# Optimization experiments

Hardware: AMD Instinct MI355X
Metric: run time of the kernel (lower is better)

## Reference

```python
import jax, jax.numpy as jnp
import numpy as np
from jax import lax

B, L, F, H, K = 16, 512, 384, 384, 3
MAX_OUT = 4096  # static upper bound on sum of durations (L * (fill_max-1) = 3584)
EPS = 1e-5
PAD = K // 2


def setup_inputs() -> dict:
    key = jax.random.key(0)
    ks = jax.random.split(key, 6)
    s = 0.02
    return {
        "input": jax.random.normal(ks[0], (B, L, F), jnp.float32),
        "target": jax.random.randint(ks[1], (B, L), 0, 8, jnp.int32),
        "conv1_w": jax.random.normal(ks[2], (H, F, K), jnp.float32) * s,
        "conv1_b": jnp.zeros((H,), jnp.float32),
        "ln1_g": jnp.ones((H,), jnp.float32),
        "ln1_b": jnp.zeros((H,), jnp.float32),
        "conv2_w": jax.random.normal(ks[3], (F, H, K), jnp.float32) * s,
        "conv2_b": jnp.zeros((F,), jnp.float32),
        "ln2_g": jnp.ones((F,), jnp.float32),
        "ln2_b": jnp.zeros((F,), jnp.float32),
        "lin_w": jax.random.normal(ks[4], (F, 1), jnp.float32) * s,
        "lin_b": jnp.zeros((1,), jnp.float32),
    }


def _conv1d(x, w, b):
    # x: [B, L, Cin] -> [B, L, Cout]; w: [Cout, Cin, K] (torch Conv1d layout)
    y = lax.conv_general_dilated(
        x.transpose(0, 2, 1), w, window_strides=(1,), padding=[(PAD, PAD)],
        dimension_numbers=("NCH", "OIH", "NCH"))
    return y.transpose(0, 2, 1) + b


def _layer_norm(x, g, b):
    mu = jnp.mean(x, axis=-1, keepdims=True)
    var = jnp.mean(jnp.square(x - mu), axis=-1, keepdims=True)
    return (x - mu) * lax.rsqrt(var + EPS) * g + b


def _length_regulate(x, dur_int):
    # cumsum-based index mapping + gather (vectorized LR_function)
    ends = jnp.cumsum(dur_int, axis=-1)                      # [B, L]
    ts = jnp.arange(MAX_OUT)                                 # [T]
    idx = jax.vmap(lambda e: jnp.searchsorted(e, ts, side="right"))(ends)  # [B, T]
    gathered = jnp.take_along_axis(x, jnp.clip(idx, 0, L - 1)[:, :, None], axis=1)
    mask = (ts[None, :] < ends[:, -1:]).astype(x.dtype)      # zero-pad past total length
    return gathered * mask[:, :, None]


def reference(input, target, conv1_w, conv1_b, ln1_g, ln1_b,
              conv2_w, conv2_b, ln2_g, ln2_b, lin_w, lin_b):
    # DurationPredictor (eval mode: dropout is identity)
    h = jax.nn.relu(_layer_norm(_conv1d(input, conv1_w, conv1_b), ln1_g, ln1_b))
    h = jax.nn.relu(_layer_norm(_conv1d(h, conv2_w, conv2_b), ln2_g, ln2_b))
    durations = jnp.exp(jax.nn.relu(h @ lin_w + lin_b))       # [B, L, 1]
    # LR_function with target durations (round of int target is identity)
    out = _length_regulate(input, target)                      # [B, MAX_OUT, F]
    return out, durations
```

## Files before the change

### kernel.cpp

```cpp
#include <hip/hip_runtime.h>
#include <math.h>

#define B_ 16
#define L_ 512
#define F_ 384
#define H_ 384
#define K_ 3
#define MAX_OUT_ 4096
#define EPS_ 1e-5f

#define M_TOTAL (B_ * L_)
#define KDIM (K_ * F_)
#define NMB 128
#define NCG 6
#define NST 36
#define APANEL (66 * 64)
#define AMBLK (12 * APANEL)
#define APLANE (NMB * AMBLK)
#define BSTEP 4096
#define BCG (NST * BSTEP)
#define BPLANE (NCG * BCG)

typedef __attribute__((ext_vector_type(8))) short bf16x8;
typedef __attribute__((ext_vector_type(4))) float f32x4;

__device__ inline unsigned short bf16_rne(float v) {
    unsigned int u = __float_as_uint(v);
    unsigned int r = (u + 0x7fffu + ((u >> 16) & 1u)) >> 16;
    return (unsigned short)r;
}
__device__ inline void bf16_split(float v, unsigned short& hi, unsigned short& lo) {
    hi = bf16_rne(v);
    float hf = __uint_as_float(((unsigned int)hi) << 16);
    lo = bf16_rne(v - hf);
}

__global__ void k_scan_prep(const int* __restrict__ target, int* __restrict__ idx,
                            const float* __restrict__ x,
                            const float* __restrict__ w1, const float* __restrict__ w2,
                            unsigned short* __restrict__ aph, unsigned short* __restrict__ apl,
                            unsigned short* __restrict__ b1h, unsigned short* __restrict__ b1l,
                            unsigned short* __restrict__ b2h, unsigned short* __restrict__ b2l) {
    if (blockIdx.x < 16) {
        __shared__ int e[L_];
        const int b = blockIdx.x;
        const int tid = threadIdx.x;
        e[tid] = target[b * L_ + tid];
        __syncthreads();
        for (int off = 1; off < L_; off <<= 1) {
            int add = (tid >= off) ? e[tid - off] : 0;
            __syncthreads();
            e[tid] += add;
            __syncthreads();
        }
        const int total = e[L_ - 1];
        for (int t = tid; t < MAX_OUT_; t += L_) {
            int lo = 0, hi = L_;
            while (lo < hi) {
                int m = (lo + hi) >> 1;
                if (e[m] <= t) lo = m + 1; else hi = m;
            }
            int v = (t < total) ? min(lo, L_ - 1) : -1;
            idx[b * MAX_OUT_ + t] = v;
        }
        return;
    }
    const int NA8 = NMB * 12 * 66 * 4;
    const int NB8 = NCG * NST * 64 * 4;
    const int total = NA8 + 2 * NB8;
    for (int i = (blockIdx.x - 16) * blockDim.x + threadIdx.x; i < total;
         i += (gridDim.x - 16) * blockDim.x) {
        if (i < NA8) {
            const int m = i / 3168;
            int r1 = i - m * 3168;
            const int fs = r1 / 264;
            int r2 = r1 - fs * 264;
            const int rp = r2 >> 2;
            const int p = r2 & 3;
            const int cgk = p ^ ((rp >> 1) & 3);
            const int f0 = fs * 32 + cgk * 8;
            const int ll = ((m & 7) << 6) + rp - 1;
            ushort4 h0 = {0,0,0,0}, h1 = {0,0,0,0}, l0 = {0,0,0,0}, l1 = {0,0,0,0};
            if (ll >= 0 && ll < L_) {
                const float* src = x + ((size_t)((m >> 3) * L_ + ll) * F_ + f0);
                float4 va = ((const float4*)src)[0];
                float4 vb = ((const float4*)src)[1];
                bf16_split(va.x, h0.x, l0.x); bf16_split(va.y, h0.y, l0.y);
                bf16_split(va.z, h0.z, l0.z); bf16_split(va.w, h0.w, l0.w);
                bf16_split(vb.x, h1.x, l1.x); bf16_split(vb.y, h1.y, l1.y);
                bf16_split(vb.z, h1.z, l1.z); bf16_split(vb.w, h1.w, l1.w);
            }
            ((ushort4*)aph)[i * 2] = h0;  ((ushort4*)aph)[i * 2 + 1] = h1;
            ((ushort4*)apl)[i * 2] = l0;  ((ushort4*)apl)[i * 2 + 1] = l1;
        } else {
            int j = i - NA8;
            const int conv = j / NB8;
            int j2 = j - conv * NB8;
            const float* w = conv ? w2 : w1;
            unsigned short* bh = conv ? b2h : b1h;
            unsigned short* bl = conv ? b2l : b1l;
            const int cg = j2 / 9216;
            int r1 = j2 - cg * 9216;
            const int s = r1 / 256;
            int r2 = r1 - s * 256;
            const int rc = r2 >> 2;
            const int p = r2 & 3;
            const int tap = s / 12;
            const int fs = s - tap * 12;
            const int cgk = p ^ ((rc >> 1) & 3);
            const int f0 = fs * 32 + cgk * 8;
            const int h = cg * 64 + rc;
            ushort4 hv0, hv1, lv0, lv1;
            unsigned short th, tl;
#define WSPLIT(E, DH, DL) bf16_split(w[(size_t)(h * F_ + f0 + (E)) * K_ + tap], th, tl); DH = th; DL = tl;
            WSPLIT(0, hv0.x, lv0.x) WSPLIT(1, hv0.y, lv0.y)
            WSPLIT(2, hv0.z, lv0.z) WSPLIT(3, hv0.w, lv0.w)
            WSPLIT(4, hv1.x, lv1.x) WSPLIT(5, hv1.y, lv1.y)
            WSPLIT(6, hv1.z, lv1.z) WSPLIT(7, hv1.w, lv1.w)
#undef WSPLIT
            ((ushort4*)bh)[j2 * 2] = hv0;  ((ushort4*)bh)[j2 * 2 + 1] = hv1;
            ((ushort4*)bl)[j2 * 2] = lv0;  ((ushort4*)bl)[j2 * 2 + 1] = lv1;
        }
    }
}

typedef __attribute__((address_space(3))) char lds_char;
typedef const __attribute__((address_space(1))) char g_char;

#define GLDS(gsrc, ldst)                                                   \
    __builtin_amdgcn_global_load_lds((g_char*)(gsrc), (lds_char*)(ldst), 16, 0, 0)

#define ST(S) {                                                            \
    const int off = wvA ? ((((S) % 12) * 66 + (S) / 12) * 64) : ((S) * 4096); \
    _Pragma("unroll")                                                      \
    for (int q = 0; q < 4; ++q)                                            \
        GLDS(srcbase + off + q * 1024,                                     \
             smem + ((S) % 3) * 16384 + wvoff + q * 1024);                 \
}

#define MFMA1(A, Bv, MI, NI)                                               \
    acc[MI][NI] = __builtin_amdgcn_mfma_f32_16x16x32_bf16(A, Bv, acc[MI][NI], 0, 0, 0);

#define STEP(S, NW, DOSTAGE) {                                             \
    asm volatile("s_waitcnt vmcnt(" #NW ")" ::: "memory");                 \
    __builtin_amdgcn_s_barrier();                                          \
    const char* bb = smem + ((S) % 3) * 16384;                             \
    const int tp = (S) / 12;                                               \
    bf16x8 ah0 = *(const bf16x8*)(bb + aadr0[tp]);                         \
    bf16x8 ah1 = *(const bf16x8*)(bb + aadr1[tp]);                         \
    bf16x8 al0 = *(const bf16x8*)(bb + 4096 + aadr0[tp]);                  \
    bf16x8 al1 = *(const bf16x8*)(bb + 4096 + aadr1[tp]);                  \
    bf16x8 bh0 = *(const bf16x8*)(bb + 8192 + badr0);                      \
    bf16x8 bh1 = *(const bf16x8*)(bb + 8192 + badr1);                      \
    bf16x8 bl0 = *(const bf16x8*)(bb + 12288 + badr0);                     \
    bf16x8 bl1 = *(const bf16x8*)(bb + 12288 + badr1);                     \
    DOSTAGE;                                                               \
    asm volatile("s_waitcnt lgkmcnt(0)" ::: "memory");                     \
    __builtin_amdgcn_sched_barrier(0);                                     \
    __builtin_amdgcn_s_setprio(1);                                         \
    MFMA1(ah0, bh0, 0, 0) MFMA1(ah0, bh1, 0, 1)                            \
    MFMA1(ah1, bh0, 1, 0) MFMA1(ah1, bh1, 1, 1)                            \
    MFMA1(ah0, bl0, 0, 0) MFMA1(ah0, bl1, 0, 1)                            \
    MFMA1(ah1, bl0, 1, 0) MFMA1(ah1, bl1, 1, 1)                            \
    MFMA1(al0, bh0, 0, 0) MFMA1(al0, bh1, 0, 1)                            \
    MFMA1(al1, bh0, 1, 0) MFMA1(al1, bh1, 1, 1)                            \
    __builtin_amdgcn_s_setprio(0);                                         \
}

__global__ __launch_bounds__(256, 3) void k_gemm(
        const unsigned short* __restrict__ Aph,
        const unsigned short* __restrict__ Apl,
        const unsigned short* __restrict__ Bph,
        const unsigned short* __restrict__ Bpl,
        float* __restrict__ C) {
    __shared__ __align__(1024) char smem[49152];
    const int lane = threadIdx.x & 63;
    const int wv = threadIdx.x >> 6;
    const int wr = wv >> 1;
    const int wc = wv & 1;
    const int m = blockIdx.x;
    const int cg = blockIdx.y;
    const int r0 = m * 64;
    const int h0 = cg * 64;

    const bool wvA = (wv < 2);
    const int wvoff = wv * 4096;
    const char* srcbase;
    {
        const char* ap = (wv == 0) ? (const char*)Aph : (const char*)Apl;
        const char* bp = (wv == 2) ? (const char*)Bph : (const char*)Bpl;
        srcbase = (wvA ? ap + (size_t)m * AMBLK : bp + (size_t)cg * BCG) + lane * 16;
    }

    const int fr = lane & 15;
    const int fc = lane >> 4;
    const int rowA0 = wr * 32 + fr, rowA1 = rowA0 + 16;
    const int colB0 = wc * 32 + fr, colB1 = colB0 + 16;
    int aadr0[3], aadr1[3];
#pragma unroll
    for (int t = 0; t < 3; ++t) {
        aadr0[t] = rowA0 * 64 + ((fc ^ (((rowA0 + t) >> 1) & 3)) << 4);
        aadr1[t] = rowA1 * 64 + ((fc ^ (((rowA1 + t) >> 1) & 3)) << 4);
    }
    const int badr0 = colB0 * 64 + ((fc ^ ((colB0 >> 1) & 3)) << 4);
    const int badr1 = colB1 * 64 + ((fc ^ ((colB1 >> 1) & 3)) << 4);

    const f32x4 z4 = {0.f, 0.f, 0.f, 0.f};
    f32x4 acc[2][2];
    acc[0][0] = z4; acc[0][1] = z4; acc[1][0] = z4; acc[1][1] = z4;

    ST(0) ST(1)

    STEP(0, 4, ST(2))   STEP(1, 4, ST(3))   STEP(2, 4, ST(4))
    STEP(3, 4, ST(5))   STEP(4, 4, ST(6))   STEP(5, 4, ST(7))
    STEP(6, 4, ST(8))   STEP(7, 4, ST(9))   STEP(8, 4, ST(10))
    STEP(9, 4, ST(11))  STEP(10, 4, ST(12)) STEP(11, 4, ST(13))
    STEP(12, 4, ST(14)) STEP(13, 4, ST(15)) STEP(14, 4, ST(16))
    STEP(15, 4, ST(17)) STEP(16, 4, ST(18)) STEP(17, 4, ST(19))
    STEP(18, 4, ST(20)) STEP(19, 4, ST(21)) STEP(20, 4, ST(22))
    STEP(21, 4, ST(23)) STEP(22, 4, ST(24)) STEP(23, 4, ST(25))
    STEP(24, 4, ST(26)) STEP(25, 4, ST(27)) STEP(26, 4, ST(28))
    STEP(27, 4, ST(29)) STEP(28, 4, ST(30)) STEP(29, 4, ST(31))
    STEP(30, 4, ST(32)) STEP(31, 4, ST(33)) STEP(32, 4, ST(34))
    STEP(33, 4, ST(35)) STEP(34, 4, )       STEP(35, 0, )

    const int rb = (lane >> 4) * 4;
#pragma unroll
    for (int mi = 0; mi < 2; ++mi)
#pragma unroll
        for (int ni = 0; ni < 2; ++ni)
#pragma unroll
            for (int r = 0; r < 4; ++r)
                C[(size_t)(r0 + wr * 32 + mi * 16 + rb + r) * H_ +
                  h0 + wc * 32 + ni * 16 + fr] = acc[mi][ni][r];
}

__global__ __launch_bounds__(256) void k_lnrelu(
        const float* __restrict__ c, const float* __restrict__ cb,
        const float* __restrict__ g, const float* __restrict__ bt,
        unsigned short* __restrict__ oh, unsigned short* __restrict__ ol) {
    const int row = blockIdx.x * 4 + (threadIdx.x >> 6);
    const int lane = threadIdx.x & 63;
    const float* cr = c + (size_t)row * H_;
    float2 dv[3];
    dv[0] = ((const float2*)cr)[lane];
    dv[1] = ((const float2*)cr)[lane + 64];
    dv[2] = ((const float2*)cr)[lane + 128];
#pragma unroll
    for (int p = 0; p < 3; ++p) {
        const int ch = 2 * (lane + 64 * p);
        dv[p].x += cb[ch];
        dv[p].y += cb[ch + 1];
    }
    float s = dv[0].x + dv[0].y + dv[1].x + dv[1].y + dv[2].x + dv[2].y;
    float s2 = dv[0].x * dv[0].x + dv[0].y * dv[0].y + dv[1].x * dv[1].x
             + dv[1].y * dv[1].y + dv[2].x * dv[2].x + dv[2].y * dv[2].y;
    for (int off = 32; off >= 1; off >>= 1) {
        s += __shfl_xor(s, off);
        s2 += __shfl_xor(s2, off);
    }
    const float mu = s * (1.f / H_);
    const float var = s2 * (1.f / H_) - mu * mu;
    const float rs = rsqrtf(var + EPS_);
    unsigned short hv[6], lv[6];
#pragma unroll
    for (int p = 0; p < 3; ++p) {
        const int ch = 2 * (lane + 64 * p);
        float r0 = fmaxf((dv[p].x - mu) * rs * g[ch] + bt[ch], 0.f);
        float r1 = fmaxf((dv[p].y - mu) * rs * g[ch + 1] + bt[ch + 1], 0.f);
        bf16_split(r0, hv[2 * p], lv[2 * p]);
        bf16_split(r1, hv[2 * p + 1], lv[2 * p + 1]);
    }
#define WSLOT(M, RP) {                                                        \
    _Pragma("unroll")                                                         \
    for (int p = 0; p < 3; ++p) {                                             \
        const int ch = 2 * (lane + 64 * p);                                   \
        const int fs = ch >> 5;                                               \
        const int k32 = ch & 31;                                              \
        const int pst = (k32 >> 3) ^ (((RP) >> 1) & 3);                       \
        const size_t ix = ((size_t)(((M) * 12 + fs) * 66 + (RP)) * 4 + pst) * 8 + (k32 & 7); \
        *(ushort2*)(oh + ix) = make_ushort2(hv[2 * p], hv[2 * p + 1]);        \
        *(ushort2*)(ol + ix) = make_ushort2(lv[2 * p], lv[2 * p + 1]);        \
    }                                                                         \
}
    const int m1 = row >> 6;
    const int rsub = row & 63;
    WSLOT(m1, rsub + 1);
    if (rsub == 0 && (row & 511) != 0)   WSLOT(m1 - 1, 65);
    if (rsub == 63 && (row & 511) != 511) WSLOT(m1 + 1, 0);
#undef WSLOT
}

__global__ __launch_bounds__(256) void k_fin_gather(
        const float* __restrict__ c, const float* __restrict__ cb,
        const float* __restrict__ g, const float* __restrict__ bt,
        const float* __restrict__ lw, const float* __restrict__ lb,
        float* __restrict__ dur,
        const float4* __restrict__ x, const int* __restrict__ idx,
        float4* __restrict__ out) {
    if (blockIdx.x < 2048) {
        const int row = blockIdx.x * 4 + (threadIdx.x >> 6);
        const int lane = threadIdx.x & 63;
        const float* cr = c + (size_t)row * F_;
        float2 dv[3];
        dv[0] = ((const float2*)cr)[lane];
        dv[1] = ((const float2*)cr)[lane + 64];
        dv[2] = ((const float2*)cr)[lane + 128];
#pragma unroll
        for (int p = 0; p < 3; ++p) {
            const int ch = 2 * (lane + 64 * p);
            dv[p].x += cb[ch];
            dv[p].y += cb[ch + 1];
        }
        float s = dv[0].x + dv[0].y + dv[1].x + dv[1].y + dv[2].x + dv[2].y;
        float s2 = dv[0].x * dv[0].x + dv[0].y * dv[0].y + dv[1].x * dv[1].x
                 + dv[1].y * dv[1].y + dv[2].x * dv[2].x + dv[2].y * dv[2].y;
        for (int off = 32; off >= 1; off >>= 1) {
            s += __shfl_xor(s, off);
            s2 += __shfl_xor(s2, off);
        }
        const float mu = s * (1.f / F_);
        const float var = s2 * (1.f / F_) - mu * mu;
        const float rs = rsqrtf(var + EPS_);
        float dot = 0.f;
#pragma unroll
        for (int p = 0; p < 3; ++p) {
            const int ch = 2 * (lane + 64 * p);
            float r0 = fmaxf((dv[p].x - mu) * rs * g[ch] + bt[ch], 0.f);
            float r1 = fmaxf((dv[p].y - mu) * rs * g[ch + 1] + bt[ch + 1], 0.f);
            dot += r0 * lw[ch] + r1 * lw[ch + 1];
        }
        for (int off = 32; off >= 1; off >>= 1) dot += __shfl_xor(dot, off);
        if (lane == 0) dur[row] = expf(fmaxf(dot + lb[0], 0.f));
    }
    const int F4 = F_ / 4;
    const int total = B_ * MAX_OUT_ * F4;
    for (int i = blockIdx.x * blockDim.x + threadIdx.x; i < total;
         i += gridDim.x * blockDim.x) {
        int row = i / F4;
        int f4 = i - row * F4;
        int t = row % MAX_OUT_;
        int b = row / MAX_OUT_;
        int id = idx[b * MAX_OUT_ + t];
        float4 v = make_float4(0.f, 0.f, 0.f, 0.f);
        if (id >= 0) v = x[((size_t)b * L_ + id) * F4 + f4];
        out[i] = v;
    }
}

extern "C" void kernel_launch(void* const* d_in, const int* in_sizes, int n_in,
                              void* d_out, int out_size, void* d_ws, size_t ws_size,
                              hipStream_t stream) {
    const float* input   = (const float*)d_in[0];
    const int*   target  = (const int*)d_in[1];
    const float* conv1_w = (const float*)d_in[2];
    const float* conv1_b = (const float*)d_in[3];
    const float* ln1_g   = (const float*)d_in[4];
    const float* ln1_b   = (const float*)d_in[5];
    const float* conv2_w = (const float*)d_in[6];
    const float* conv2_b = (const float*)d_in[7];
    const float* ln2_g   = (const float*)d_in[8];
    const float* ln2_b   = (const float*)d_in[9];
    const float* lin_w   = (const float*)d_in[10];
    const float* lin_b   = (const float*)d_in[11];

    float* out0 = (float*)d_out;
    float* dur  = out0 + (size_t)B_ * MAX_OUT_ * F_;
    char* ob = (char*)d_out;
    unsigned short* aph = (unsigned short*)(ob + (16u << 20));
    unsigned short* apl = (unsigned short*)(ob + (24u << 20));

    char* ws = (char*)d_ws;
    int* idx = (int*)ws;
    unsigned short* b1h = (unsigned short*)(ws + 262144);
    unsigned short* b1l = b1h + BPLANE / 2;
    unsigned short* b2h = b1l + BPLANE / 2;
    unsigned short* b2l = b2h + BPLANE / 2;
    float* c = (float*)(ws + 262144 + 4 * (size_t)BPLANE);

    hipLaunchKernelGGL(k_scan_prep, dim3(1040), dim3(512), 0, stream,
                       target, idx, input, conv1_w, conv2_w,
                       aph, apl, b1h, b1l, b2h, b2l);
    hipLaunchKernelGGL(k_gemm, dim3(NMB, NCG), dim3(256), 0, stream,
                       aph, apl, b1h, b1l, c);
    hipLaunchKernelGGL(k_lnrelu, dim3(M_TOTAL / 4), dim3(256), 0, stream,
                       c, conv1_b, ln1_g, ln1_b, aph, apl);
    hipLaunchKernelGGL(k_gemm, dim3(NMB, NCG), dim3(256), 0, stream,
                       aph, apl, b2h, b2l, c);
    hipLaunchKernelGGL(k_fin_gather, dim3(4096), dim3(256), 0, stream,
                       c, conv2_b, ln2_g, ln2_b, lin_w, lin_b, dur,
                       (const float4*)input, idx, (float4*)out0);
}
```

Before: 89.88 us.

## Coalesce weight prepack reads and stagger LDS waits to overlap with MFMAs

```diff
diff --git a/kernel.cpp b/kernel.cpp
--- a/kernel.cpp
+++ b/kernel.cpp
@@ -66,8 +66,8 @@
         return;
     }
     const int NA8 = NMB * 12 * 66 * 4;
-    const int NB8 = NCG * NST * 64 * 4;
-    const int total = NA8 + 2 * NB8;
+    const int NW2 = 2 * H_ * 48;
+    const int total = NA8 + NW2;
     for (int i = (blockIdx.x - 16) * blockDim.x + threadIdx.x; i < total;
          i += (gridDim.x - 16) * blockDim.x) {
         if (i < NA8) {
@@ -93,33 +93,43 @@
             ((ushort4*)aph)[i * 2] = h0;  ((ushort4*)aph)[i * 2 + 1] = h1;
             ((ushort4*)apl)[i * 2] = l0;  ((ushort4*)apl)[i * 2 + 1] = l1;
         } else {
-            int j = i - NA8;
-            const int conv = j / NB8;
-            int j2 = j - conv * NB8;
+            const int j = i - NA8;
+            const int conv = j / (H_ * 48);
+            const int j2 = j - conv * (H_ * 48);
+            const int h = j2 / 48;
+            const int oct = j2 - h * 48;
             const float* w = conv ? w2 : w1;
             unsigned short* bh = conv ? b2h : b1h;
             unsigned short* bl = conv ? b2l : b1l;
-            const int cg = j2 / 9216;
-            int r1 = j2 - cg * 9216;
-            const int s = r1 / 256;
-            int r2 = r1 - s * 256;
-            const int rc = r2 >> 2;
-            const int p = r2 & 3;
-            const int tap = s / 12;
-            const int fs = s - tap * 12;
-            const int cgk = p ^ ((rc >> 1) & 3);
-            const int f0 = fs * 32 + cgk * 8;
-            const int h = cg * 64 + rc;
-            ushort4 hv0, hv1, lv0, lv1;
-            unsigned short th, tl;
-#define WSPLIT(E, DH, DL) bf16_split(w[(size_t)(h * F_ + f0 + (E)) * K_ + tap], th, tl); DH = th; DL = tl;
-            WSPLIT(0, hv0.x, lv0.x) WSPLIT(1, hv0.y, lv0.y)
-            WSPLIT(2, hv0.z, lv0.z) WSPLIT(3, hv0.w, lv0.w)
-            WSPLIT(4, hv1.x, lv1.x) WSPLIT(5, hv1.y, lv1.y)
-            WSPLIT(6, hv1.z, lv1.z) WSPLIT(7, hv1.w, lv1.w)
-#undef WSPLIT
-            ((ushort4*)bh)[j2 * 2] = hv0;  ((ushort4*)bh)[j2 * 2 + 1] = hv1;
-            ((ushort4*)bl)[j2 * 2] = lv0;  ((ushort4*)bl)[j2 * 2 + 1] = lv1;
+            const float4* wp = (const float4*)(w + ((size_t)h * F_ + oct * 8) * K_);
+            float v[24];
+#pragma unroll
+            for (int q = 0; q < 6; ++q) {
+                float4 t4 = wp[q];
+                v[q * 4] = t4.x; v[q * 4 + 1] = t4.y;
+                v[q * 4 + 2] = t4.z; v[q * 4 + 3] = t4.w;
+            }
+            const int cg = h >> 6;
+            const int rc = h & 63;
+            const int fs = oct >> 2;
+            const int cgk = oct & 3;
+            const int pst = cgk ^ ((rc >> 1) & 3);
+#pragma unroll
+            for (int tap = 0; tap < 3; ++tap) {
+                ushort4 hv0, hv1, lv0, lv1;
+                bf16_split(v[0 * 3 + tap], hv0.x, lv0.x);
+                bf16_split(v[1 * 3 + tap], hv0.y, lv0.y);
+                bf16_split(v[2 * 3 + tap], hv0.z, lv0.z);
+                bf16_split(v[3 * 3 + tap], hv0.w, lv0.w);
+                bf16_split(v[4 * 3 + tap], hv1.x, lv1.x);
+                bf16_split(v[5 * 3 + tap], hv1.y, lv1.y);
+                bf16_split(v[6 * 3 + tap], hv1.z, lv1.z);
+                bf16_split(v[7 * 3 + tap], hv1.w, lv1.w);
+                const int s = tap * 12 + fs;
+                const int ci = ((cg * 36 + s) * 64 + rc) * 4 + pst;
+                ((ushort4*)bh)[ci * 2] = hv0;  ((ushort4*)bh)[ci * 2 + 1] = hv1;
+                ((ushort4*)bl)[ci * 2] = lv0;  ((ushort4*)bl)[ci * 2 + 1] = lv1;
+            }
         }
     }
 }
@@ -140,6 +150,8 @@
 
 #define MFMA1(A, Bv, MI, NI)                                               \
     acc[MI][NI] = __builtin_amdgcn_mfma_f32_16x16x32_bf16(A, Bv, acc[MI][NI], 0, 0, 0);
+
+#define SB __builtin_amdgcn_sched_barrier(0)
 
 #define STEP(S, NW, DOSTAGE) {                                             \
     asm volatile("s_waitcnt vmcnt(" #NW ")" ::: "memory");                 \
@@ -148,20 +160,27 @@
     const int tp = (S) / 12;                                               \
     bf16x8 ah0 = *(const bf16x8*)(bb + aadr0[tp]);                         \
     bf16x8 ah1 = *(const bf16x8*)(bb + aadr1[tp]);                         \
+    bf16x8 bh0 = *(const bf16x8*)(bb + 8192 + badr0);                      \
+    bf16x8 bh1 = *(const bf16x8*)(bb + 8192 + badr1);                      \
+    SB;                                                                    \
+    bf16x8 bl0 = *(const bf16x8*)(bb + 12288 + badr0);                     \
+    bf16x8 bl1 = *(const bf16x8*)(bb + 12288 + badr1);                     \
+    SB;                                                                    \
     bf16x8 al0 = *(const bf16x8*)(bb + 4096 + aadr0[tp]);                  \
     bf16x8 al1 = *(const bf16x8*)(bb + 4096 + aadr1[tp]);                  \
-    bf16x8 bh0 = *(const bf16x8*)(bb + 8192 + badr0);                      \
-    bf16x8 bh1 = *(const bf16x8*)(bb + 8192 + badr1);                      \
-    bf16x8 bl0 = *(const bf16x8*)(bb + 12288 + badr0);                     \
-    bf16x8 bl1 = *(const bf16x8*)(bb + 12288 + badr1);                     \
+    SB;                                                                    \
     DOSTAGE;                                                               \
-    asm volatile("s_waitcnt lgkmcnt(0)" ::: "memory");                     \
-    __builtin_amdgcn_sched_barrier(0);                                     \
+    asm volatile("s_waitcnt lgkmcnt(4)" ::: "memory");                     \
+    SB;                                                                    \
     __builtin_amdgcn_s_setprio(1);                                         \
     MFMA1(ah0, bh0, 0, 0) MFMA1(ah0, bh1, 0, 1)                            \
     MFMA1(ah1, bh0, 1, 0) MFMA1(ah1, bh1, 1, 1)                            \
+    asm volatile("s_waitcnt lgkmcnt(2)" ::: "memory");                     \
+    SB;                                                                    \
     MFMA1(ah0, bl0, 0, 0) MFMA1(ah0, bl1, 0, 1)                            \
     MFMA1(ah1, bl0, 1, 0) MFMA1(ah1, bl1, 1, 1)                            \
+    asm volatile("s_waitcnt lgkmcnt(0)" ::: "memory");                     \
+    SB;                                                                    \
     MFMA1(al0, bh0, 0, 0) MFMA1(al0, bh1, 0, 1)                            \
     MFMA1(al1, bh0, 1, 0) MFMA1(al1, bh1, 1, 1)                            \
     __builtin_amdgcn_s_setprio(0);                                         \
```

Result: no change. 90.28 us (+0.5%).
